# Kernel optimization log

Hardware: AMD Instinct MI355X
Metric: run time of the kernel (lower is better)

## Reference

```python
import jax, jax.numpy as jnp
import numpy as np

B, S, E, M = 128, 196, 768, 768

def setup_inputs() -> dict:
    key = jax.random.key(0)
    k1, k2, k3, k4, k5 = jax.random.split(key, 5)
    sent_emb = jax.random.normal(k1, (B, S, E), dtype=jnp.float32)
    # valid event spans: start in [0, S-6), end = start + len, len in [1,5]
    starts = jax.random.randint(k2, (B, 2), 0, S - 6)
    lens = jax.random.randint(k3, (B, 2), 1, 6)
    ends = starts + lens
    batch_e = jnp.stack([starts[:, 0], ends[:, 0], starts[:, 1], ends[:, 1]], axis=1).astype(jnp.int64)
    mlp_w = jax.random.normal(k4, (M, 2 * E), dtype=jnp.float32) * 0.02
    mlp_b = jnp.zeros((M,), dtype=jnp.float32)
    fk_w = jax.random.normal(k5, (M, S * E), dtype=jnp.float32) * 0.005
    fk_b = jnp.zeros((M,), dtype=jnp.float32)
    return {"sent_emb": sent_emb, "batch_e": batch_e, "mlp_w": mlp_w,
            "mlp_b": mlp_b, "fk_w": fk_w, "fk_b": fk_b, "batch_size": B}

def reference(sent_emb, batch_e, mlp_w, mlp_b, fk_w, fk_b, batch_size):
    b, s, e = sent_emb.shape
    # sent_process: flatten each sentence's [S,E] embeddings into one row [S*E]
    sent_emb_cat = sent_emb.reshape(b, s * e)  # [B, S*E]
    # extract_event: mean-pool over the two variable-length spans (vectorized via masks)
    pos = jnp.arange(s)  # [S]
    m1 = ((pos >= batch_e[:, 0:1]) & (pos < batch_e[:, 1:2])).astype(sent_emb.dtype)  # [B,S]
    m2 = ((pos >= batch_e[:, 2:3]) & (pos < batch_e[:, 3:4])).astype(sent_emb.dtype)
    e1 = jnp.einsum('bs,bse->be', m1, sent_emb) / jnp.sum(m1, axis=1, keepdims=True)
    e2 = jnp.einsum('bs,bse->be', m2, sent_emb) / jnp.sum(m2, axis=1, keepdims=True)
    event_pair = jnp.concatenate([e1, e2], axis=1)  # [B, 2E]
    pred = 0.9 * (event_pair @ mlp_w.T + mlp_b) + 0.1 * (sent_emb_cat @ fk_w.T + fk_b)
    return pred
```

## Files before the change

kernel.cpp:

```cpp
#include <hip/hip_runtime.h>
#include <hip/hip_bf16.h>

#define B_ 128
#define S_ 196
#define E_ 768
#define M_ 768
#define KTOT (S_*E_)
#define BK 256
#define SS_TOTAL (KTOT/BK)
#define KSPLIT 42
#define SS_PER (SS_TOTAL/KSPLIT)
#define BN 48
#define MTN (M_/BN)
#define PITCH 528
#define ZC 6

typedef __bf16 bf16x8 __attribute__((ext_vector_type(8)));
typedef __bf16 bf16x4 __attribute__((ext_vector_type(4)));
typedef float  f32x4  __attribute__((ext_vector_type(4)));

__device__ inline bf16x8 cvt8(const float* __restrict__ p) {
    float4 a = *(const float4*)p;
    float4 b = *(const float4*)(p + 4);
    bf16x8 r;
    r[0] = (__bf16)a.x; r[1] = (__bf16)a.y; r[2] = (__bf16)a.z; r[3] = (__bf16)a.w;
    r[4] = (__bf16)b.x; r[5] = (__bf16)b.y; r[6] = (__bf16)b.z; r[7] = (__bf16)b.w;
    return r;
}

__global__ void init_out(const float* __restrict__ mlp_b,
                         const float* __restrict__ fk_b,
                         float* __restrict__ out) {
    int i = blockIdx.x * 256 + threadIdx.x;
    if (i < B_ * M_) {
        int m = i % M_;
        out[i] = 0.9f * mlp_b[m] + 0.1f * fk_b[m];
    }
}

__global__ void pack_a(const float* __restrict__ A, __bf16* __restrict__ Apk) {
    const int nchunk = SS_TOTAL * 8 * 8 * 64;
    for (int c = blockIdx.x * blockDim.x + threadIdx.x; c < nchunk;
         c += gridDim.x * blockDim.x) {
        int lane = c & 63;
        int kf   = (c >> 6) & 7;
        int bt   = (c >> 9) & 7;
        int ss   = c >> 12;
        int b = bt * 16 + (lane & 15);
        int k = ss * BK + kf * 32 + (lane >> 4) * 8;
        *(bf16x8*)(Apk + (size_t)c * 8) = cvt8(A + (size_t)b * KTOT + k);
    }
}

__global__ void event_pool(const float* __restrict__ SE,
                           const int* __restrict__ BE, int be_stride,
                           float* __restrict__ EP) {
    int b = blockIdx.x;
    int s1 = BE[(b*4 + 0) * be_stride];
    int e1 = BE[(b*4 + 1) * be_stride];
    int s2 = BE[(b*4 + 2) * be_stride];
    int e2 = BE[(b*4 + 3) * be_stride];
    float inv1 = 1.0f / (float)(e1 - s1);
    float inv2 = 1.0f / (float)(e2 - s2);
    for (int c = threadIdx.x; c < E_; c += 256) {
        float sum1 = 0.f, sum2 = 0.f;
        for (int s = s1; s < e1; ++s) sum1 += SE[((size_t)b * S_ + s) * E_ + c];
        for (int s = s2; s < e2; ++s) sum2 += SE[((size_t)b * S_ + s) * E_ + c];
        EP[b * (2*E_) + c]       = sum1 * inv1;
        EP[b * (2*E_) + E_ + c]  = sum2 * inv2;
    }
}

__global__ __launch_bounds__(256) void mlp_gemm(const float* __restrict__ EP,
                                                const float* __restrict__ Wm,
                                                float* __restrict__ out) {
    const int wid   = (blockIdx.x * 256 + threadIdx.x) >> 6;
    const int lane  = threadIdx.x & 63;
    const int bt    = wid & 7;
    const int mt    = wid >> 3;
    const int row16 = lane & 15;
    const int kgrp  = lane >> 4;
    const float* Arow = EP + (size_t)(bt*16 + row16) * (2*E_);
    const float* Brow = Wm + (size_t)(mt*16 + row16) * (2*E_);
    f32x4 acc = {};
    for (int k0 = 0; k0 < 2*E_; k0 += 32) {
        bf16x8 af = cvt8(Arow + k0 + kgrp*8);
        bf16x8 bv = cvt8(Brow + k0 + kgrp*8);
        acc = __builtin_amdgcn_mfma_f32_16x16x32_bf16(af, bv, acc, 0, 0, 0);
    }
    const int m = mt*16 + row16;
#pragma unroll
    for (int r = 0; r < 4; ++r) {
        const int b = bt*16 + kgrp*4 + r;
        out[b * M_ + m] += 0.9f * acc[r];
    }
}


#define LOAD_A(AREG, sl)                                                      \
    _Pragma("unroll")                                                         \
    for (int kf = 0; kf < 8; ++kf)                                            \
        AREG[kf] = *(const bf16x8*)(abase + (size_t)(sl) * 32768 + kf * 512);

#define LOAD_W(sl)                                                            \
    _Pragma("unroll")                                                         \
    for (int i = 0; i < 6; ++i)                                               \
        wr[i] = *(const float4*)(wbase + (size_t)i * KTOT + (size_t)(sl) * BK);

#define WRITE_W(buf)                                                          \
    _Pragma("unroll")                                                         \
    for (int i = 0; i < 6; ++i) {                                             \
        bf16x4 h;                                                             \
        h[0] = (__bf16)wr[i].x; h[1] = (__bf16)wr[i].y;                       \
        h[2] = (__bf16)wr[i].z; h[3] = (__bf16)wr[i].w;                       \
        *(bf16x4*)(&Wlds[buf][0] + wb + i * PITCH) = h;                       \
    }

#define COMPUTE(AREG, buf)                                                    \
    _Pragma("unroll")                                                         \
    for (int kf = 0; kf < 8; ++kf) {                                          \
        _Pragma("unroll")                                                     \
        for (int n = 0; n < 3; ++n) {                                         \
            bf16x8 wf = *(const bf16x8*)(&Wlds[buf][0] +                      \
                        (n * 16 + r16) * PITCH + kf * 64 + kg * 16);          \
            acc[n] = __builtin_amdgcn_mfma_f32_16x16x32_bf16(AREG[kf], wf,    \
                                                             acc[n], 0, 0, 0);\
        }                                                                     \
    }

__global__ __launch_bounds__(512, 4) void fk_gemm(const __bf16* __restrict__ Apk,
                                                  const float* __restrict__ W,
                                                  float* __restrict__ partial) {
    __shared__ __align__(16) char Wlds[2][BN * PITCH];

    const int wg = blockIdx.x;
    const int mt = wg % MTN;
    const int kz = wg / MTN;
    const int ss0 = kz * SS_PER;

    const int tid = threadIdx.x;
    const int wv  = tid >> 6;
    const int lane = tid & 63;
    const int r16 = lane & 15;
    const int kg  = lane >> 4;

    const float*  wbase = W + (size_t)(mt * BN + wv * 6) * KTOT
                            + (size_t)ss0 * BK + lane * 4;
    const int     wb    = (wv * 6) * PITCH + lane * 8;
    const __bf16* abase = Apk + ((size_t)ss0 * 8 + wv) * 4096 + lane * 8;

    f32x4 acc[3] = {};
    float4 wr[6];
    bf16x8 aA[8], aB[8];

    LOAD_W(0)
    LOAD_A(aA, 0)
    WRITE_W(0)
    __syncthreads();

#pragma unroll
    for (int p = 0; p < SS_PER / 2; ++p) {
        LOAD_W(2 * p + 1)
        LOAD_A(aB, 2 * p + 1)
        COMPUTE(aA, 0)
        WRITE_W(1)
        __syncthreads();
        if (p < SS_PER / 2 - 1) {
            LOAD_W(2 * p + 2)
            LOAD_A(aA, 2 * p + 2)
        }
        COMPUTE(aB, 1)
        if (p < SS_PER / 2 - 1) {
            WRITE_W(0)
        }
        __syncthreads();
    }

    float* pz = partial + (size_t)kz * (B_ * M_);
#pragma unroll
    for (int n = 0; n < 3; ++n) {
        const int m = mt * BN + n * 16 + r16;
#pragma unroll
        for (int r = 0; r < 4; ++r) {
            const int b = wv * 16 + kg * 4 + r;
            pz[(size_t)b * M_ + m] = acc[n][r];
        }
    }
}

__global__ void reduce_k(const float* __restrict__ pp, float* __restrict__ out) {
    int t = blockIdx.x * 256 + threadIdx.x;
    int i = t % (B_ * M_);
    int zc = t / (B_ * M_);
    if (zc >= ZC) return;
    float s = 0.f;
#pragma unroll
    for (int z = zc * (KSPLIT / ZC); z < (zc + 1) * (KSPLIT / ZC); ++z)
        s += pp[(size_t)z * (B_ * M_) + i];
    atomicAdd(out + i, 0.1f * s);
}

extern "C" void kernel_launch(void* const* d_in, const int* in_sizes, int n_in,
                              void* d_out, int out_size, void* d_ws, size_t ws_size,
                              hipStream_t stream) {
    const float* se    = (const float*)d_in[0];
    const int*   be    = (const int*)  d_in[1];
    const float* mlp_w = (const float*)d_in[2];
    const float* mlp_b = (const float*)d_in[3];
    const float* fk_w  = (const float*)d_in[4];
    const float* fk_b  = (const float*)d_in[5];
    float* out = (float*)d_out;
    float* ep  = (float*)d_ws;
    float* pp  = ep + (size_t)B_ * 2 * E_;
    __bf16* apk = (__bf16*)(pp + (size_t)KSPLIT * B_ * M_);

    const int be_stride = (in_sizes[1] == B_ * 4 * 2) ? 2 : 1;

    init_out<<<(B_ * M_ + 255) / 256, 256, 0, stream>>>(mlp_b, fk_b, out);
    pack_a<<<3072, 256, 0, stream>>>(se, apk);
    event_pool<<<B_, 256, 0, stream>>>(se, be, be_stride, ep);
    mlp_gemm<<<(B_ / 16) * (M_ / 16) / 4, 256, 0, stream>>>(ep, mlp_w, out);
    fk_gemm<<<MTN * KSPLIT, 512, 0, stream>>>(apk, fk_w, pp);
    reduce_k<<<(B_ * M_ * ZC + 255) / 256, 256, 0, stream>>>(pp, out);
}
```

Measured before the change: 189.4 us.

## Fuse prep and epilogue kernels and shrink split-K to 32 slices

Merges init_out, event pooling and A-packing into one prep launch, and merges the split-K reduction with the small MLP GEMM into one post launch that uses atomics for both contributions. KSPLIT drops from 42 to 32 with uneven per-slice K ranges, giving 512 GEMM workgroups and fewer partial buffers to write and reduce. The fk_gemm main loop is rewritten with two W register sets and a single A register set loaded just before compute, with a tail for odd slice counts. The aim is to cut launch count, partial-sum traffic and register pressure. The trade-off is less prefetch of A ahead of compute, a longer per-workgroup K loop, and atomic adds from the MLP path.

```diff
diff --git a/kernel.cpp b/kernel.cpp
--- a/kernel.cpp
+++ b/kernel.cpp
@@ -8,12 +8,11 @@
 #define KTOT (S_*E_)
 #define BK 256
 #define SS_TOTAL (KTOT/BK)
-#define KSPLIT 42
-#define SS_PER (SS_TOTAL/KSPLIT)
+#define KSPLIT 32
 #define BN 48
 #define MTN (M_/BN)
 #define PITCH 528
-#define ZC 6
+#define ZC 4
 
 typedef __bf16 bf16x8 __attribute__((ext_vector_type(8)));
 typedef __bf16 bf16x4 __attribute__((ext_vector_type(4)));
@@ -28,71 +27,44 @@
     return r;
 }
 
-__global__ void init_out(const float* __restrict__ mlp_b,
-                         const float* __restrict__ fk_b,
-                         float* __restrict__ out) {
-    int i = blockIdx.x * 256 + threadIdx.x;
-    if (i < B_ * M_) {
+__global__ void prep(const float* __restrict__ mlp_b,
+                     const float* __restrict__ fk_b,
+                     const float* __restrict__ A,
+                     const int* __restrict__ BE, int be_stride,
+                     float* __restrict__ out,
+                     float* __restrict__ EP,
+                     __bf16* __restrict__ Apk) {
+    const int bid = blockIdx.x;
+    if (bid < 384) {
+        int i = bid * 256 + threadIdx.x;
         int m = i % M_;
         out[i] = 0.9f * mlp_b[m] + 0.1f * fk_b[m];
-    }
-}
-
-__global__ void pack_a(const float* __restrict__ A, __bf16* __restrict__ Apk) {
-    const int nchunk = SS_TOTAL * 8 * 8 * 64;
-    for (int c = blockIdx.x * blockDim.x + threadIdx.x; c < nchunk;
-         c += gridDim.x * blockDim.x) {
-        int lane = c & 63;
-        int kf   = (c >> 6) & 7;
-        int bt   = (c >> 9) & 7;
-        int ss   = c >> 12;
-        int b = bt * 16 + (lane & 15);
-        int k = ss * BK + kf * 32 + (lane >> 4) * 8;
-        *(bf16x8*)(Apk + (size_t)c * 8) = cvt8(A + (size_t)b * KTOT + k);
-    }
-}
-
-__global__ void event_pool(const float* __restrict__ SE,
-                           const int* __restrict__ BE, int be_stride,
-                           float* __restrict__ EP) {
-    int b = blockIdx.x;
-    int s1 = BE[(b*4 + 0) * be_stride];
-    int e1 = BE[(b*4 + 1) * be_stride];
-    int s2 = BE[(b*4 + 2) * be_stride];
-    int e2 = BE[(b*4 + 3) * be_stride];
-    float inv1 = 1.0f / (float)(e1 - s1);
-    float inv2 = 1.0f / (float)(e2 - s2);
-    for (int c = threadIdx.x; c < E_; c += 256) {
-        float sum1 = 0.f, sum2 = 0.f;
-        for (int s = s1; s < e1; ++s) sum1 += SE[((size_t)b * S_ + s) * E_ + c];
-        for (int s = s2; s < e2; ++s) sum2 += SE[((size_t)b * S_ + s) * E_ + c];
-        EP[b * (2*E_) + c]       = sum1 * inv1;
-        EP[b * (2*E_) + E_ + c]  = sum2 * inv2;
-    }
-}
-
-__global__ __launch_bounds__(256) void mlp_gemm(const float* __restrict__ EP,
-                                                const float* __restrict__ Wm,
-                                                float* __restrict__ out) {
-    const int wid   = (blockIdx.x * 256 + threadIdx.x) >> 6;
-    const int lane  = threadIdx.x & 63;
-    const int bt    = wid & 7;
-    const int mt    = wid >> 3;
-    const int row16 = lane & 15;
-    const int kgrp  = lane >> 4;
-    const float* Arow = EP + (size_t)(bt*16 + row16) * (2*E_);
-    const float* Brow = Wm + (size_t)(mt*16 + row16) * (2*E_);
-    f32x4 acc = {};
-    for (int k0 = 0; k0 < 2*E_; k0 += 32) {
-        bf16x8 af = cvt8(Arow + k0 + kgrp*8);
-        bf16x8 bv = cvt8(Brow + k0 + kgrp*8);
-        acc = __builtin_amdgcn_mfma_f32_16x16x32_bf16(af, bv, acc, 0, 0, 0);
-    }
-    const int m = mt*16 + row16;
-#pragma unroll
-    for (int r = 0; r < 4; ++r) {
-        const int b = bt*16 + kgrp*4 + r;
-        out[b * M_ + m] += 0.9f * acc[r];
+    } else if (bid < 512) {
+        int b = bid - 384;
+        int s1 = BE[(b*4 + 0) * be_stride];
+        int e1 = BE[(b*4 + 1) * be_stride];
+        int s2 = BE[(b*4 + 2) * be_stride];
+        int e2 = BE[(b*4 + 3) * be_stride];
+        float inv1 = 1.0f / (float)(e1 - s1);
+        float inv2 = 1.0f / (float)(e2 - s2);
+        for (int c = threadIdx.x; c < E_; c += 256) {
+            float sum1 = 0.f, sum2 = 0.f;
+            for (int s = s1; s < e1; ++s) sum1 += A[((size_t)b * S_ + s) * E_ + c];
+            for (int s = s2; s < e2; ++s) sum2 += A[((size_t)b * S_ + s) * E_ + c];
+            EP[b * (2*E_) + c]       = sum1 * inv1;
+            EP[b * (2*E_) + E_ + c]  = sum2 * inv2;
+        }
+    } else {
+        const int nchunk = SS_TOTAL * 8 * 8 * 64;
+        for (int c = (bid - 512) * 256 + threadIdx.x; c < nchunk; c += 3072 * 256) {
+            int lane = c & 63;
+            int kf   = (c >> 6) & 7;
+            int bt   = (c >> 9) & 7;
+            int ss   = c >> 12;
+            int b = bt * 16 + (lane & 15);
+            int k = ss * BK + kf * 32 + (lane >> 4) * 8;
+            *(bf16x8*)(Apk + (size_t)c * 8) = cvt8(A + (size_t)b * KTOT + k);
+        }
     }
 }
 
@@ -102,17 +74,17 @@
     for (int kf = 0; kf < 8; ++kf)                                            \
         AREG[kf] = *(const bf16x8*)(abase + (size_t)(sl) * 32768 + kf * 512);
 
-#define LOAD_W(sl)                                                            \
+#define LOAD_W(WREG, sl)                                                      \
     _Pragma("unroll")                                                         \
     for (int i = 0; i < 6; ++i)                                               \
-        wr[i] = *(const float4*)(wbase + (size_t)i * KTOT + (size_t)(sl) * BK);
-
-#define WRITE_W(buf)                                                          \
+        WREG[i] = *(const float4*)(wbase + (size_t)i * KTOT + (size_t)(sl) * BK);
+
+#define WRITE_W(WREG, buf)                                                    \
     _Pragma("unroll")                                                         \
     for (int i = 0; i < 6; ++i) {                                             \
         bf16x4 h;                                                             \
-        h[0] = (__bf16)wr[i].x; h[1] = (__bf16)wr[i].y;                       \
-        h[2] = (__bf16)wr[i].z; h[3] = (__bf16)wr[i].w;                       \
+        h[0] = (__bf16)WREG[i].x; h[1] = (__bf16)WREG[i].y;                   \
+        h[2] = (__bf16)WREG[i].z; h[3] = (__bf16)WREG[i].w;                   \
         *(bf16x4*)(&Wlds[buf][0] + wb + i * PITCH) = h;                       \
     }
 
@@ -134,9 +106,10 @@
     __shared__ __align__(16) char Wlds[2][BN * PITCH];
 
     const int wg = blockIdx.x;
-    const int mt = wg % MTN;
-    const int kz = wg / MTN;
-    const int ss0 = kz * SS_PER;
+    const int mt = wg & (MTN - 1);
+    const int kz = wg >> 4;
+    const int ss0 = (SS_TOTAL * kz) / KSPLIT;
+    const int SSN = (SS_TOTAL * (kz + 1)) / KSPLIT - ss0;
 
     const int tid = threadIdx.x;
     const int wv  = tid >> 6;
@@ -150,30 +123,34 @@
     const __bf16* abase = Apk + ((size_t)ss0 * 8 + wv) * 4096 + lane * 8;
 
     f32x4 acc[3] = {};
-    float4 wr[6];
-    bf16x8 aA[8], aB[8];
-
-    LOAD_W(0)
-    LOAD_A(aA, 0)
-    WRITE_W(0)
+    float4 w0[6], w1[6];
+    bf16x8 aA[8];
+
+    LOAD_W(w0, 0)
+    WRITE_W(w0, 0)
+    LOAD_W(w1, 1)
     __syncthreads();
 
-#pragma unroll
-    for (int p = 0; p < SS_PER / 2; ++p) {
-        LOAD_W(2 * p + 1)
-        LOAD_A(aB, 2 * p + 1)
+    int sl = 0;
+    for (; sl + 2 < SSN; sl += 2) {
+        LOAD_A(aA, sl)
+        LOAD_W(w0, sl + 2)
         COMPUTE(aA, 0)
-        WRITE_W(1)
+        WRITE_W(w1, 1)
         __syncthreads();
-        if (p < SS_PER / 2 - 1) {
-            LOAD_W(2 * p + 2)
-            LOAD_A(aA, 2 * p + 2)
-        }
-        COMPUTE(aB, 1)
-        if (p < SS_PER / 2 - 1) {
-            WRITE_W(0)
-        }
+        LOAD_A(aA, sl + 1)
+        if (sl + 3 < SSN) { LOAD_W(w1, sl + 3) }
+        COMPUTE(aA, 1)
+        WRITE_W(w0, 0)
         __syncthreads();
+    }
+    LOAD_A(aA, sl)
+    COMPUTE(aA, 0)
+    if (SSN - sl == 2) {
+        WRITE_W(w1, 1)
+        __syncthreads();
+        LOAD_A(aA, sl + 1)
+        COMPUTE(aA, 1)
     }
 
     float* pz = partial + (size_t)kz * (B_ * M_);
@@ -188,16 +165,42 @@
     }
 }
 
-__global__ void reduce_k(const float* __restrict__ pp, float* __restrict__ out) {
-    int t = blockIdx.x * 256 + threadIdx.x;
-    int i = t % (B_ * M_);
-    int zc = t / (B_ * M_);
-    if (zc >= ZC) return;
-    float s = 0.f;
-#pragma unroll
-    for (int z = zc * (KSPLIT / ZC); z < (zc + 1) * (KSPLIT / ZC); ++z)
-        s += pp[(size_t)z * (B_ * M_) + i];
-    atomicAdd(out + i, 0.1f * s);
+__global__ __launch_bounds__(256) void post(const float* __restrict__ pp,
+                                            const float* __restrict__ EP,
+                                            const float* __restrict__ Wm,
+                                            float* __restrict__ out) {
+    const int bid = blockIdx.x;
+    if (bid < 1536) {
+        int t = bid * 256 + threadIdx.x;
+        int i = t % (B_ * M_);
+        int zc = t / (B_ * M_);
+        float s = 0.f;
+#pragma unroll
+        for (int z = zc * (KSPLIT / ZC); z < (zc + 1) * (KSPLIT / ZC); ++z)
+            s += pp[(size_t)z * (B_ * M_) + i];
+        atomicAdd(out + i, 0.1f * s);
+    } else {
+        const int wid   = ((bid - 1536) * 256 + threadIdx.x) >> 6;
+        const int lane  = threadIdx.x & 63;
+        const int bt    = wid & 7;
+        const int mt    = wid >> 3;
+        const int row16 = lane & 15;
+        const int kgrp  = lane >> 4;
+        const float* Arow = EP + (size_t)(bt*16 + row16) * (2*E_);
+        const float* Brow = Wm + (size_t)(mt*16 + row16) * (2*E_);
+        f32x4 acc = {};
+        for (int k0 = 0; k0 < 2*E_; k0 += 32) {
+            bf16x8 af = cvt8(Arow + k0 + kgrp*8);
+            bf16x8 bv = cvt8(Brow + k0 + kgrp*8);
+            acc = __builtin_amdgcn_mfma_f32_16x16x32_bf16(af, bv, acc, 0, 0, 0);
+        }
+        const int m = mt*16 + row16;
+#pragma unroll
+        for (int r = 0; r < 4; ++r) {
+            const int b = bt*16 + kgrp*4 + r;
+            atomicAdd(out + b * M_ + m, 0.9f * acc[r]);
+        }
+    }
 }
 
 extern "C" void kernel_launch(void* const* d_in, const int* in_sizes, int n_in,
@@ -216,10 +219,7 @@
 
     const int be_stride = (in_sizes[1] == B_ * 4 * 2) ? 2 : 1;
 
-    init_out<<<(B_ * M_ + 255) / 256, 256, 0, stream>>>(mlp_b, fk_b, out);
-    pack_a<<<3072, 256, 0, stream>>>(se, apk);
-    event_pool<<<B_, 256, 0, stream>>>(se, be, be_stride, ep);
-    mlp_gemm<<<(B_ / 16) * (M_ / 16) / 4, 256, 0, stream>>>(ep, mlp_w, out);
+    prep<<<3584, 256, 0, stream>>>(mlp_b, fk_b, se, be, be_stride, out, ep, apk);
     fk_gemm<<<MTN * KSPLIT, 512, 0, stream>>>(apk, fk_w, pp);
-    reduce_k<<<(B_ * M_ * ZC + 255) / 256, 256, 0, stream>>>(pp, out);
-}
+    post<<<1632, 256, 0, stream>>>(pp, ep, mlp_w, out);
+}
```

New measurement: 172.9 us. 8.7% less time.
